# Kernel optimization log

Hardware: AMD Instinct MI355X
Metric: run time of the kernel (lower is better)

## Reference

```python
import jax, jax.numpy as jnp
import numpy as np
import math

N = 50000        # nodes
E = 800000       # edges (avg degree 16)
F_IN = 128
F_OUT = 64


def setup_inputs() -> dict:
    key = jax.random.key(0)
    k = jax.random.split(key, 7)
    stdv = 1.0 / math.sqrt(F_OUT)
    x = jax.random.normal(k[0], (N, F_IN), dtype=jnp.float32)
    t = jax.random.uniform(k[1], (N,), dtype=jnp.float32)
    src = jax.random.randint(k[2], (E,), 0, N, dtype=jnp.int64)
    dst = jax.random.randint(k[3], (E,), 0, N, dtype=jnp.int64)
    # sparse adjacency values (e.g. normalized adjacency weights)
    edge_vals = jax.random.uniform(k[4], (E,), dtype=jnp.float32)
    weight = jax.random.uniform(k[5], (F_IN, F_OUT), dtype=jnp.float32,
                                minval=-stdv, maxval=stdv)
    bias = jax.random.uniform(k[6], (F_OUT,), dtype=jnp.float32,
                              minval=-stdv, maxval=stdv)
    return {"x": x, "t": t, "src": src, "dst": dst,
            "edge_vals": edge_vals, "weight": weight, "bias": bias}


def reference(x, t, src, dst, edge_vals, weight, bias):
    # support = (X @ W) * t[:, None]   -- dense GEMM + per-row scale
    support = (x @ weight) * t[:, None]                 # [N, F_OUT]
    # spmm(adj, support): gather rows at src, scale by edge value, reduce by dst
    msgs = support[src] * edge_vals[:, None]            # [E, F_OUT]
    out = jax.ops.segment_sum(msgs, dst, num_segments=N)  # [N, F_OUT]
    return out + bias
```

## Files before the change

kernel.cpp:

```cpp
#include <hip/hip_runtime.h>
#include <hip/hip_bf16.h>

#define FIN 128
#define FOUT 64
#define TILE_ROWS 64

#define EPB 2048
#define NPB 32
#define NBUK_MAX 1600
#define CAP 768

#define OFF_CUR   6400000
#define OFF_OVFC  6406400
#define OFF_TMP   6406464
#define OFF_OVF   16236864

typedef short bf16x8 __attribute__((ext_vector_type(8)));
typedef float f32x4  __attribute__((ext_vector_type(4)));

__device__ inline ushort f32_to_bf16_rne(float f) {
    unsigned u = __float_as_uint(f);
    u += 0x7FFFu + ((u >> 16) & 1u);
    return (ushort)(u >> 16);
}
__device__ inline float bf16_to_f32(ushort h) {
    return __uint_as_float((unsigned)h << 16);
}

union __align__(16) K1Sh {
    ushort wt[FOUT * FIN];
    struct { int h[NBUK_MAX]; int c[NBUK_MAX]; } sc;
};

__global__ __launch_bounds__(256) void gemm_scatter_kernel(
    const float* __restrict__ x, const float* __restrict__ t,
    const float* __restrict__ W, ushort* __restrict__ support, int N,
    const int* __restrict__ src, const int* __restrict__ dst,
    const float* __restrict__ ev, int* __restrict__ cur,
    int2* __restrict__ tmp, int* __restrict__ ovfc, int4* __restrict__ ovf,
    int E, int SBP, int NBUK, int GB)
{
    __shared__ K1Sh sh;
    const int tid = threadIdx.x;

    if (blockIdx.x >= (unsigned)GB) {
        const int chunk = blockIdx.x - GB;
        const int e0    = chunk * EPB;

        for (int i = tid; i < NBUK; i += 256) sh.sc.h[i] = 0;
        __syncthreads();

        for (int i = tid; i < EPB; i += 256) {
            int e = e0 + i;
            if (e < E) atomicAdd(&sh.sc.h[dst[e] >> 5], 1);
        }
        __syncthreads();

        for (int j = tid; j < NBUK; j += 256) {
            int hj = sh.sc.h[j];
            if (hj) sh.sc.c[j] = atomicAdd(&cur[j], hj);
        }
        __syncthreads();

        for (int i = tid; i < EPB; i += 256) {
            int e = e0 + i;
            if (e < E) {
                int d = dst[e];
                int j = d >> 5;
                int s = atomicAdd(&sh.sc.c[j], 1);
                int2 rec = make_int2(src[e] | ((d & (NPB - 1)) << 16),
                                     __float_as_int(ev[e]));
                if (s < CAP) {
                    tmp[(size_t)j * CAP + s] = rec;
                } else {
                    int o = atomicAdd(ovfc, 1);
                    if (o < E) ovf[o] = make_int4(rec.x, rec.y, j, 0);
                }
            }
        }
        return;
    }

    const int gb   = blockIdx.x;
    const int lane = tid & 63;
    const int w    = tid >> 6;
    const int ln   = lane & 15;
    const int q    = lane >> 4;
    const int rowb = gb * TILE_ROWS + w * 16;
    const int arow = rowb + ln;

    for (int idx = tid; idx < FIN * FOUT; idx += 256) {
        int k = idx >> 6;
        int n = idx & 63;
        sh.wt[n * FIN + (k ^ ((n & 7) << 3))] = f32_to_bf16_rne(W[idx]);
    }
    __syncthreads();

    f32x4 acc[4];
    #pragma unroll
    for (int nt = 0; nt < 4; ++nt)
        #pragma unroll
        for (int r = 0; r < 4; ++r) acc[nt][r] = 0.f;

    const bool aok = (arow < N);
    const float* xrow = &x[(size_t)arow * FIN];

    #pragma unroll
    for (int kc = 0; kc < 4; ++kc) {
        float xs[8];
        #pragma unroll
        for (int j = 0; j < 8; ++j) xs[j] = 0.f;
        if (aok) {
            float4 x0 = *(const float4*)&xrow[kc * 32 + q * 8];
            float4 x1 = *(const float4*)&xrow[kc * 32 + q * 8 + 4];
            xs[0] = x0.x; xs[1] = x0.y; xs[2] = x0.z; xs[3] = x0.w;
            xs[4] = x1.x; xs[5] = x1.y; xs[6] = x1.z; xs[7] = x1.w;
        }
        bf16x8 a;
        #pragma unroll
        for (int j = 0; j < 8; ++j) a[j] = (short)f32_to_bf16_rne(xs[j]);

        const int k0 = kc * 32 + q * 8;
        #pragma unroll
        for (int nt = 0; nt < 4; ++nt) {
            bf16x8 b = *(const bf16x8*)
                &sh.wt[(nt * 16 + ln) * FIN + (k0 ^ ((ln & 7) << 3))];
            acc[nt] = __builtin_amdgcn_mfma_f32_16x16x32_bf16(a, b, acc[nt], 0, 0, 0);
        }
    }

    #pragma unroll
    for (int reg = 0; reg < 4; ++reg) {
        int r = rowb + q * 4 + reg;
        if (r < N) {
            float tv = t[r];
            #pragma unroll
            for (int nt = 0; nt < 4; ++nt)
                support[(size_t)r * FOUT + nt * 16 + ln] =
                    f32_to_bf16_rne(acc[nt][reg] * tv);
        }
    }
}

__global__ __launch_bounds__(256) void bucket_gather_kernel(
    const int* __restrict__ curg, const int2* __restrict__ tmp,
    const ushort* __restrict__ support, const float* __restrict__ bias,
    float* __restrict__ out, const int* __restrict__ ovfc,
    const int4* __restrict__ ovf, int E, int N, int NBUK)
{
    __shared__ int2 raw[CAP];
    __shared__ int2 sorted[CAP];
    __shared__ int  cnt[NPB];
    __shared__ int  starts[NPB + 1];
    __shared__ int  cur[NPB];
    __shared__ int  novs;

    const int tid   = threadIdx.x;
    const int w     = tid >> 6;
    const int lane  = tid & 63;
    const int B     = blockIdx.x;
    const int node0 = B * NPB;

    const int base   = B * CAP;
    const int tot    = curg[B];
    const int placed = (tot < CAP) ? tot : CAP;

    if (tid < NPB) cnt[tid] = 0;
    __syncthreads();

    for (int i = tid; i < placed; i += 256) {
        int2 r = tmp[base + i];
        raw[i] = r;
        atomicAdd(&cnt[(r.x >> 16) & (NPB - 1)], 1);
    }
    __syncthreads();

    if (tid < 64) {
        int v   = (tid < NPB) ? cnt[tid] : 0;
        int val = v;
        #pragma unroll
        for (int d = 1; d < NPB; d <<= 1) {
            int n = __shfl_up(val, d);
            if (tid >= d) val += n;
        }
        if (tid < NPB) {
            starts[tid] = val - v;
            cur[tid]    = val - v;
        }
        if (tid == 0) starts[NPB] = placed;
    }
    __syncthreads();

    for (int i = tid; i < placed; i += 256) {
        int2 r  = raw[i];
        int pos = atomicAdd(&cur[(r.x >> 16) & (NPB - 1)], 1);
        sorted[pos] = r;
    }
    __syncthreads();

    const int fl = lane & 15;
    const int g  = lane >> 4;
    const float4 bv4 = *(const float4*)&bias[fl * 4];

    for (int nn = 0; nn < 8; ++nn) {
        const int nl = w * 8 + nn;
        const int rb = starts[nl];
        const int re = starts[nl + 1];

        float a0 = 0.f, a1 = 0.f, a2 = 0.f, a3 = 0.f;
        for (int i = rb + g; i < re; i += 4) {
            int2 r = sorted[i];
            uint2 u = *(const uint2*)
                &support[(size_t)(r.x & 0xFFFF) * FOUT + fl * 4];
            float wg = __int_as_float(r.y);
            a0 += bf16_to_f32((ushort)(u.x & 0xFFFFu)) * wg;
            a1 += bf16_to_f32((ushort)(u.x >> 16)) * wg;
            a2 += bf16_to_f32((ushort)(u.y & 0xFFFFu)) * wg;
            a3 += bf16_to_f32((ushort)(u.y >> 16)) * wg;
        }
        #pragma unroll
        for (int d = 16; d < 64; d <<= 1) {
            a0 += __shfl_xor(a0, d);
            a1 += __shfl_xor(a1, d);
            a2 += __shfl_xor(a2, d);
            a3 += __shfl_xor(a3, d);
        }
        const int node = node0 + nl;
        if (g == 0 && node < N) {
            float4 o;
            o.x = a0 + bv4.x; o.y = a1 + bv4.y;
            o.z = a2 + bv4.z; o.w = a3 + bv4.w;
            *(float4*)&out[(size_t)node * FOUT + fl * 4] = o;
        }
    }

    __syncthreads();
    if (tid == 0) novs = *ovfc;
    __syncthreads();
    int nov = novs;
    if (nov > 0) {
        if (nov > E) nov = E;
        __threadfence();
        for (int k = w; k < nov; k += 4) {
            int4 r = ovf[k];
            if (r.z == B) {
                int node = node0 + ((r.x >> 16) & (NPB - 1));
                if (node < N) {
                    float v = bf16_to_f32(
                        support[(size_t)(r.x & 0xFFFF) * FOUT + lane]);
                    atomicAdd(&out[(size_t)node * FOUT + lane],
                              v * __int_as_float(r.y));
                }
            }
        }
    }
}

extern "C" void kernel_launch(void* const* d_in, const int* in_sizes, int n_in,
                              void* d_out, int out_size, void* d_ws, size_t ws_size,
                              hipStream_t stream) {
    const float* x    = (const float*)d_in[0];
    const float* t    = (const float*)d_in[1];
    const int*   src  = (const int*)d_in[2];
    const int*   dst  = (const int*)d_in[3];
    const float* ev   = (const float*)d_in[4];
    const float* W    = (const float*)d_in[5];
    const float* bias = (const float*)d_in[6];
    float* out = (float*)d_out;

    const int N = in_sizes[1];
    const int E = in_sizes[2];

    char*   ws      = (char*)d_ws;
    ushort* support = (ushort*)ws;
    int*    cur     = (int*)(ws + OFF_CUR);
    int*    ovfc    = (int*)(ws + OFF_OVFC);
    int2*   tmp     = (int2*)(ws + OFF_TMP);
    int4*   ovf     = (int4*)(ws + OFF_OVF);

    const int GB   = (N + TILE_ROWS - 1) / TILE_ROWS;
    const int SBP  = (E + EPB - 1) / EPB;
    const int NBUK = (N + NPB - 1) / NPB;

    hipMemsetAsync(ws + OFF_CUR, 0, OFF_TMP - OFF_CUR, stream);

    gemm_scatter_kernel<<<GB + SBP, 256, 0, stream>>>(
        x, t, W, support, N, src, dst, ev, cur, tmp, ovfc, ovf,
        E, SBP, NBUK, GB);

    bucket_gather_kernel<<<NBUK, 256, 0, stream>>>(
        cur, tmp, support, bias, out, ovfc, ovf, E, N, NBUK);
}
```

Measured before the change: 132.5 us.

## Replace in-block counting sort with LDS float atomic accumulation per node

```diff
diff --git a/kernel.cpp b/kernel.cpp
--- a/kernel.cpp
+++ b/kernel.cpp
@@ -9,6 +9,7 @@
 #define NPB 32
 #define NBUK_MAX 1600
 #define CAP 768
+#define ACCS 68
 
 #define OFF_CUR   6400000
 #define OFF_OVFC  6406400
@@ -148,16 +149,12 @@
     float* __restrict__ out, const int* __restrict__ ovfc,
     const int4* __restrict__ ovf, int E, int N, int NBUK)
 {
-    __shared__ int2 raw[CAP];
-    __shared__ int2 sorted[CAP];
-    __shared__ int  cnt[NPB];
-    __shared__ int  starts[NPB + 1];
-    __shared__ int  cur[NPB];
-    __shared__ int  novs;
+    __shared__ float acc[NPB * ACCS];
+    __shared__ int novs;
 
     const int tid   = threadIdx.x;
-    const int w     = tid >> 6;
-    const int lane  = tid & 63;
+    const int g     = tid >> 4;
+    const int fl    = tid & 15;
     const int B     = blockIdx.x;
     const int node0 = B * NPB;
 
@@ -165,72 +162,67 @@
     const int tot    = curg[B];
     const int placed = (tot < CAP) ? tot : CAP;
 
-    if (tid < NPB) cnt[tid] = 0;
-    __syncthreads();
-
-    for (int i = tid; i < placed; i += 256) {
+    for (int i = tid; i < NPB * ACCS; i += 256) acc[i] = 0.f;
+    __syncthreads();
+
+    int i = g;
+    for (; i + 48 < placed; i += 64) {
+        int2 r0 = tmp[base + i];
+        int2 r1 = tmp[base + i + 16];
+        int2 r2 = tmp[base + i + 32];
+        int2 r3 = tmp[base + i + 48];
+        uint2 u0 = *(const uint2*)&support[(size_t)(r0.x & 0xFFFF) * FOUT + fl * 4];
+        uint2 u1 = *(const uint2*)&support[(size_t)(r1.x & 0xFFFF) * FOUT + fl * 4];
+        uint2 u2 = *(const uint2*)&support[(size_t)(r2.x & 0xFFFF) * FOUT + fl * 4];
+        uint2 u3 = *(const uint2*)&support[(size_t)(r3.x & 0xFFFF) * FOUT + fl * 4];
+        float w0 = __int_as_float(r0.y), w1 = __int_as_float(r1.y);
+        float w2 = __int_as_float(r2.y), w3 = __int_as_float(r3.y);
+        float* a0 = &acc[((r0.x >> 16) & (NPB - 1)) * ACCS + fl * 4];
+        float* a1 = &acc[((r1.x >> 16) & (NPB - 1)) * ACCS + fl * 4];
+        float* a2 = &acc[((r2.x >> 16) & (NPB - 1)) * ACCS + fl * 4];
+        float* a3 = &acc[((r3.x >> 16) & (NPB - 1)) * ACCS + fl * 4];
+        atomicAdd(&a0[0], bf16_to_f32((ushort)(u0.x & 0xFFFFu)) * w0);
+        atomicAdd(&a0[1], bf16_to_f32((ushort)(u0.x >> 16)) * w0);
+        atomicAdd(&a0[2], bf16_to_f32((ushort)(u0.y & 0xFFFFu)) * w0);
+        atomicAdd(&a0[3], bf16_to_f32((ushort)(u0.y >> 16)) * w0);
+        atomicAdd(&a1[0], bf16_to_f32((ushort)(u1.x & 0xFFFFu)) * w1);
+        atomicAdd(&a1[1], bf16_to_f32((ushort)(u1.x >> 16)) * w1);
+        atomicAdd(&a1[2], bf16_to_f32((ushort)(u1.y & 0xFFFFu)) * w1);
+        atomicAdd(&a1[3], bf16_to_f32((ushort)(u1.y >> 16)) * w1);
+        atomicAdd(&a2[0], bf16_to_f32((ushort)(u2.x & 0xFFFFu)) * w2);
+        atomicAdd(&a2[1], bf16_to_f32((ushort)(u2.x >> 16)) * w2);
+        atomicAdd(&a2[2], bf16_to_f32((ushort)(u2.y & 0xFFFFu)) * w2);
+        atomicAdd(&a2[3], bf16_to_f32((ushort)(u2.y >> 16)) * w2);
+        atomicAdd(&a3[0], bf16_to_f32((ushort)(u3.x & 0xFFFFu)) * w3);
+        atomicAdd(&a3[1], bf16_to_f32((ushort)(u3.x >> 16)) * w3);
+        atomicAdd(&a3[2], bf16_to_f32((ushort)(u3.y & 0xFFFFu)) * w3);
+        atomicAdd(&a3[3], bf16_to_f32((ushort)(u3.y >> 16)) * w3);
+    }
+    for (; i < placed; i += 16) {
         int2 r = tmp[base + i];
-        raw[i] = r;
-        atomicAdd(&cnt[(r.x >> 16) & (NPB - 1)], 1);
-    }
-    __syncthreads();
-
-    if (tid < 64) {
-        int v   = (tid < NPB) ? cnt[tid] : 0;
-        int val = v;
-        #pragma unroll
-        for (int d = 1; d < NPB; d <<= 1) {
-            int n = __shfl_up(val, d);
-            if (tid >= d) val += n;
-        }
-        if (tid < NPB) {
-            starts[tid] = val - v;
-            cur[tid]    = val - v;
-        }
-        if (tid == 0) starts[NPB] = placed;
-    }
-    __syncthreads();
-
-    for (int i = tid; i < placed; i += 256) {
-        int2 r  = raw[i];
-        int pos = atomicAdd(&cur[(r.x >> 16) & (NPB - 1)], 1);
-        sorted[pos] = r;
-    }
-    __syncthreads();
-
-    const int fl = lane & 15;
-    const int g  = lane >> 4;
-    const float4 bv4 = *(const float4*)&bias[fl * 4];
-
-    for (int nn = 0; nn < 8; ++nn) {
-        const int nl = w * 8 + nn;
-        const int rb = starts[nl];
-        const int re = starts[nl + 1];
-
-        float a0 = 0.f, a1 = 0.f, a2 = 0.f, a3 = 0.f;
-        for (int i = rb + g; i < re; i += 4) {
-            int2 r = sorted[i];
-            uint2 u = *(const uint2*)
-                &support[(size_t)(r.x & 0xFFFF) * FOUT + fl * 4];
-            float wg = __int_as_float(r.y);
-            a0 += bf16_to_f32((ushort)(u.x & 0xFFFFu)) * wg;
-            a1 += bf16_to_f32((ushort)(u.x >> 16)) * wg;
-            a2 += bf16_to_f32((ushort)(u.y & 0xFFFFu)) * wg;
-            a3 += bf16_to_f32((ushort)(u.y >> 16)) * wg;
-        }
-        #pragma unroll
-        for (int d = 16; d < 64; d <<= 1) {
-            a0 += __shfl_xor(a0, d);
-            a1 += __shfl_xor(a1, d);
-            a2 += __shfl_xor(a2, d);
-            a3 += __shfl_xor(a3, d);
-        }
+        uint2 u = *(const uint2*)&support[(size_t)(r.x & 0xFFFF) * FOUT + fl * 4];
+        float wg = __int_as_float(r.y);
+        float* a = &acc[((r.x >> 16) & (NPB - 1)) * ACCS + fl * 4];
+        atomicAdd(&a[0], bf16_to_f32((ushort)(u.x & 0xFFFFu)) * wg);
+        atomicAdd(&a[1], bf16_to_f32((ushort)(u.x >> 16)) * wg);
+        atomicAdd(&a[2], bf16_to_f32((ushort)(u.y & 0xFFFFu)) * wg);
+        atomicAdd(&a[3], bf16_to_f32((ushort)(u.y >> 16)) * wg);
+    }
+    __syncthreads();
+
+    {
+        const int nl   = tid >> 3;
+        const int f0   = (tid & 7) * 8;
         const int node = node0 + nl;
-        if (g == 0 && node < N) {
-            float4 o;
-            o.x = a0 + bv4.x; o.y = a1 + bv4.y;
-            o.z = a2 + bv4.z; o.w = a3 + bv4.w;
-            *(float4*)&out[(size_t)node * FOUT + fl * 4] = o;
+        if (node < N) {
+            const float* a  = &acc[nl * ACCS + f0];
+            float4 o0, o1;
+            o0.x = a[0] + bias[f0 + 0]; o0.y = a[1] + bias[f0 + 1];
+            o0.z = a[2] + bias[f0 + 2]; o0.w = a[3] + bias[f0 + 3];
+            o1.x = a[4] + bias[f0 + 4]; o1.y = a[5] + bias[f0 + 5];
+            o1.z = a[6] + bias[f0 + 6]; o1.w = a[7] + bias[f0 + 7];
+            *(float4*)&out[(size_t)node * FOUT + f0]     = o0;
+            *(float4*)&out[(size_t)node * FOUT + f0 + 4] = o1;
         }
     }
 
@@ -241,6 +233,8 @@
     if (nov > 0) {
         if (nov > E) nov = E;
         __threadfence();
+        const int w    = tid >> 6;
+        const int lane = tid & 63;
         for (int k = w; k < nov; k += 4) {
             int4 r = ovf[k];
             if (r.z == B) {
```

After: 411.9 us. +211.0%, slower.
